# Kernel tuning notes

Hardware: AMD Instinct MI355X
Metric: run time of the kernel (lower is better)

The kernel has to match this reference:

```python
import jax, jax.numpy as jnp
import numpy as np

TEMPERATURE = 0.07


def setup_inputs() -> dict:
    key = jax.random.key(0)
    k1, k2 = jax.random.split(key)
    embeddings = jax.random.normal(k1, (8192, 256), dtype=jnp.float32)
    labels = jax.random.randint(k2, (8192,), 0, 1024, dtype=jnp.int64)
    return {"embeddings": embeddings, "labels": labels}


def reference(embeddings, labels):
    b = embeddings.shape[0]
    # L2 normalize rows (torch F.normalize uses eps=1e-12 clamp on the norm)
    norm = jnp.linalg.norm(embeddings, axis=1, keepdims=True)
    en = embeddings / jnp.maximum(norm, 1e-12)
    # [B, B] similarity scaled by temperature
    sim = jnp.matmul(en, en.T) / TEMPERATURE
    # log-softmax over rows (denominator includes the diagonal, as in the original)
    logp = jax.nn.log_softmax(sim, axis=1)
    # positive mask: same label, excluding self
    mask = (labels[:, None] == labels[None, :]) & ~jnp.eye(b, dtype=bool)
    pos_mask = mask.astype(logp.dtype)
    pos_count = pos_mask.sum(axis=1)
    pos_sum = -jnp.sum(logp * pos_mask, axis=1)
    pos_loss = jnp.where(pos_count > 0, pos_sum / jnp.maximum(pos_count, 1.0), 0.0)
    return pos_loss.mean()
```

## Files before the change

### kernel.cpp

```cpp
#include <hip/hip_runtime.h>
#include <hip/hip_bf16.h>

#define B_N 8192
#define D_K 256
#define BM  32
#define BN  128
#define JSPLIT 2
#define JSPAN (B_N / JSPLIT)
#define NTILE (JSPAN / BN)
#define INVT 14.285714285714286f

typedef __bf16 bf16x8 __attribute__((ext_vector_type(8)));
typedef float  f32x16 __attribute__((ext_vector_type(16)));

#define AS1 __attribute__((address_space(1)))
#define AS3 __attribute__((address_space(3)))

__device__ __forceinline__ unsigned short f32_to_bf16_rne(float f) {
    unsigned int u = __float_as_uint(f);
    unsigned int r = (u + 0x7FFFu + ((u >> 16) & 1u)) >> 16;
    return (unsigned short)r;
}

__global__ void zero_misc(float* out, int* hist) {
    if (threadIdx.x < 1024) hist[threadIdx.x] = 0;
    if (threadIdx.x == 0) out[0] = 0.0f;
}

__global__ void norm_kernel(const float* __restrict__ emb,
                            unsigned short* __restrict__ en,
                            const int* __restrict__ labels,
                            int* __restrict__ hist) {
    const int row = blockIdx.x;
    const int t   = threadIdx.x;
    float x  = emb[row * D_K + t];
    float ss = x * x;
    #pragma unroll
    for (int m = 32; m; m >>= 1) ss += __shfl_xor(ss, m, 64);
    __shared__ float wsum[4];
    if ((t & 63) == 0) wsum[t >> 6] = ss;
    __syncthreads();
    float tot = wsum[0] + wsum[1] + wsum[2] + wsum[3];
    float sc  = 1.0f / fmaxf(sqrtf(tot), 1e-12f);
    en[row * D_K + t] = f32_to_bf16_rne(x * sc);
    if (t == 0) atomicAdd(&hist[labels[row]], 1);
}

__launch_bounds__(256, 2)
__global__ void loss_kernel(const unsigned short* __restrict__ en,
                            const int* __restrict__ labels,
                            float* __restrict__ s_part,
                            float* __restrict__ ps_part) {
    __shared__ unsigned short Bls[BN * D_K];
    __shared__ int   Lls[BN];
    __shared__ float comb[2][4][BM];

    const int t  = threadIdx.x;
    const int l  = t & 63;
    const int w  = t >> 6;
    const int ir = l & 31;
    const int h  = l >> 5;

    const int b   = blockIdx.x;
    const int swz = (b & 7) * (gridDim.x >> 3) + (b >> 3);
    const int jsplit = swz >> 8;
    const int itile  = swz & 255;
    const int ibase  = itile * BM;
    const int j0base = jsplit * JSPAN;

    bf16x8 bi[16];
    {
        const unsigned short* ap = en + (size_t)(ibase + ir) * D_K + h * 8;
        #pragma unroll
        for (int ks = 0; ks < 16; ++ks)
            bi[ks] = *reinterpret_cast<const bf16x8*>(ap + ks * 16);
    }
    const int i_glob = ibase + ir;
    const int li = labels[i_glob];

    float s_acc = 0.0f, ps_acc = 0.0f;

    for (int it = 0; it < NTILE; ++it) {
        const int j0g = j0base + it * BN;

        __syncthreads();
        #pragma unroll
        for (int rd = 0; rd < 16; ++rd) {
            int c    = rd * 256 + t;
            int row  = c >> 5;
            int m16  = c & 31;
            int srcm = m16 ^ (row & 7);
            const unsigned short* g =
                en + (size_t)(j0g + row) * D_K + srcm * 8;
            __builtin_amdgcn_global_load_lds(
                (const AS1 void*)g,
                (AS3 void*)((unsigned short*)Bls + (size_t)c * 8), 16, 0, 0);
        }
        if (t < BN) Lls[t] = labels[j0g + t];
        __syncthreads();

        f32x16 acc;
        #pragma unroll
        for (int q = 0; q < 16; ++q) acc[q] = 0.0f;
        const int x = ir & 7;
        const char* arow = (const char*)Bls + (size_t)(w * 32 + ir) * 512;
        #pragma unroll
        for (int ks = 0; ks < 16; ++ks) {
            int chunk = ((ks << 1) | h) ^ x;
            const bf16x8 af =
                *reinterpret_cast<const bf16x8*>(arow + (chunk << 4));
            acc = __builtin_amdgcn_mfma_f32_32x32x16_bf16(af, bi[ks], acc,
                                                          0, 0, 0);
        }

        const bool dtile = (j0g == (ibase & ~(BN - 1)));
        if (dtile) {
            #pragma unroll
            for (int r = 0; r < 16; ++r) {
                int jl = w * 32 + (r & 3) + ((r >> 2) << 3) + (h << 2);
                int lj = Lls[jl];
                float dot = acc[r];
                s_acc += __expf(fmaf(dot, INVT, -INVT));
                bool mm = (lj == li) & ((j0g + jl) != i_glob);
                ps_acc += mm ? dot : 0.0f;
            }
        } else {
            #pragma unroll
            for (int r = 0; r < 16; ++r) {
                int jl = w * 32 + (r & 3) + ((r >> 2) << 3) + (h << 2);
                int lj = Lls[jl];
                float dot = acc[r];
                s_acc += __expf(fmaf(dot, INVT, -INVT));
                ps_acc += (lj == li) ? dot : 0.0f;
            }
        }
    }

    s_acc  += __shfl_xor(s_acc, 32, 64);
    ps_acc += __shfl_xor(ps_acc, 32, 64);
    if (h == 0) { comb[0][w][ir] = s_acc; comb[1][w][ir] = ps_acc; }
    __syncthreads();
    if (t < BM) {
        float st  = comb[0][0][t] + comb[0][1][t] + comb[0][2][t] + comb[0][3][t];
        float pst = comb[1][0][t] + comb[1][1][t] + comb[1][2][t] + comb[1][3][t];
        s_part[jsplit * B_N + ibase + t]  = st;
        ps_part[jsplit * B_N + ibase + t] = pst;
    }
}

__global__ void final_kernel(const float* __restrict__ s_part,
                             const float* __restrict__ ps_part,
                             const int* __restrict__ labels,
                             const int* __restrict__ hist,
                             float* __restrict__ out) {
    int i = blockIdx.x * 256 + threadIdx.x;
    float s  = s_part[i] + s_part[B_N + i];
    float ps = ps_part[i] + ps_part[B_N + i];
    int pc = hist[labels[i]] - 1;
    float lse = INVT + __logf(s);
    float loss = (pc > 0) ? (lse - ps * INVT / (float)pc) : 0.0f;
    #pragma unroll
    for (int m = 1; m < 64; m <<= 1) loss += __shfl_xor(loss, m, 64);
    __shared__ float ws4[4];
    if ((threadIdx.x & 63) == 0) ws4[threadIdx.x >> 6] = loss;
    __syncthreads();
    if (threadIdx.x == 0)
        atomicAdd(out, (ws4[0] + ws4[1] + ws4[2] + ws4[3]) * (1.0f / B_N));
}

extern "C" void kernel_launch(void* const* d_in, const int* in_sizes, int n_in,
                              void* d_out, int out_size, void* d_ws, size_t ws_size,
                              hipStream_t stream) {
    const float* emb    = (const float*)d_in[0];
    const int*   labels = (const int*)d_in[1];
    float*       out    = (float*)d_out;

    unsigned short* en  = (unsigned short*)d_ws;
    float* s_part  = (float*)((char*)d_ws + (size_t)B_N * D_K * 2);
    float* ps_part = s_part + JSPLIT * B_N;
    int*   hist    = (int*)(ps_part + JSPLIT * B_N);

    hipLaunchKernelGGL(zero_misc, dim3(1), dim3(1024), 0, stream, out, hist);
    hipLaunchKernelGGL(norm_kernel, dim3(B_N), dim3(D_K), 0, stream,
                       emb, en, labels, hist);
    hipLaunchKernelGGL(loss_kernel, dim3(256 * JSPLIT), dim3(256), 0, stream,
                       en, labels, s_part, ps_part);
    hipLaunchKernelGGL(final_kernel, dim3(B_N / 256), dim3(256), 0, stream,
                       s_part, ps_part, labels, hist, out);
}
```

Baseline: 131.1 us.

## Compute positive-pair sums via per-class centroid sums and enlarge loss tile

Replaces the per-pair positive-mask accumulation in the main loop with an algebraic identity: per-class sums of normalized embeddings are built with float atomics in the norm kernel, and each row's positive sum becomes dot(e_i, C_label) minus the self dot. The loss kernel then only accumulates the softmax denominator, using exp2 with a folded constant, and the i-tile grows to 64 rows with four j-splits so each loaded B tile feeds two MFMA passes. The norm kernel is also vectorized to four rows per block. The cost is 256 float atomics per row into the class-sum matrix, plus a zeroing pass over that matrix and rounding differences between the bf16 embeddings and the fp32 class sums.

```diff
diff --git a/kernel.cpp b/kernel.cpp
--- a/kernel.cpp
+++ b/kernel.cpp
@@ -3,15 +3,18 @@
 
 #define B_N 8192
 #define D_K 256
-#define BM  32
+#define BM  64
 #define BN  128
-#define JSPLIT 2
+#define JSPLIT 4
 #define JSPAN (B_N / JSPLIT)
 #define NTILE (JSPAN / BN)
+#define NCLS 1024
 #define INVT 14.285714285714286f
+#define C1   20.60992907f
 
 typedef __bf16 bf16x8 __attribute__((ext_vector_type(8)));
 typedef float  f32x16 __attribute__((ext_vector_type(16)));
+typedef float  f32x4  __attribute__((ext_vector_type(4)));
 
 #define AS1 __attribute__((address_space(1)))
 #define AS3 __attribute__((address_space(3)))
@@ -21,151 +24,155 @@
     unsigned int r = (u + 0x7FFFu + ((u >> 16) & 1u)) >> 16;
     return (unsigned short)r;
 }
+__device__ __forceinline__ float bf16_to_f32(unsigned short u) {
+    return __uint_as_float(((unsigned int)u) << 16);
+}
 
-__global__ void zero_misc(float* out, int* hist) {
-    if (threadIdx.x < 1024) hist[threadIdx.x] = 0;
-    if (threadIdx.x == 0) out[0] = 0.0f;
+__global__ void zero_kernel(float* __restrict__ out, int* __restrict__ hist,
+                            float* __restrict__ Cmat) {
+    int g = blockIdx.x * 256 + threadIdx.x;
+    Cmat[g] = 0.0f;
+    if (g < NCLS) hist[g] = 0;
+    if (g == 0) out[0] = 0.0f;
 }
 
 __global__ void norm_kernel(const float* __restrict__ emb,
+                            const int* __restrict__ labels,
                             unsigned short* __restrict__ en,
-                            const int* __restrict__ labels,
+                            float* __restrict__ Cmat,
                             int* __restrict__ hist) {
-    const int row = blockIdx.x;
-    const int t   = threadIdx.x;
-    float x  = emb[row * D_K + t];
-    float ss = x * x;
+    const int t = threadIdx.x;
+    const int w = t >> 6, l = t & 63;
+    const int row = blockIdx.x * 4 + w;
+    f32x4 x = *reinterpret_cast<const f32x4*>(emb + (size_t)row * D_K + l * 4);
+    float ss = x[0]*x[0] + x[1]*x[1] + x[2]*x[2] + x[3]*x[3];
     #pragma unroll
-    for (int m = 32; m; m >>= 1) ss += __shfl_xor(ss, m, 64);
-    __shared__ float wsum[4];
-    if ((t & 63) == 0) wsum[t >> 6] = ss;
-    __syncthreads();
-    float tot = wsum[0] + wsum[1] + wsum[2] + wsum[3];
-    float sc  = 1.0f / fmaxf(sqrtf(tot), 1e-12f);
-    en[row * D_K + t] = f32_to_bf16_rne(x * sc);
-    if (t == 0) atomicAdd(&hist[labels[row]], 1);
+    for (int m = 1; m < 64; m <<= 1) ss += __shfl_xor(ss, m, 64);
+    float sc = 1.0f / fmaxf(sqrtf(ss), 1e-12f);
+    const int lab = labels[row];
+    float xn[4];
+    ushort4 o;
+    #pragma unroll
+    for (int k = 0; k < 4; ++k) xn[k] = x[k] * sc;
+    o.x = f32_to_bf16_rne(xn[0]); o.y = f32_to_bf16_rne(xn[1]);
+    o.z = f32_to_bf16_rne(xn[2]); o.w = f32_to_bf16_rne(xn[3]);
+    *reinterpret_cast<ushort4*>(en + (size_t)row * D_K + l * 4) = o;
+    #pragma unroll
+    for (int k = 0; k < 4; ++k)
+        atomicAdd(&Cmat[lab * D_K + l * 4 + k], xn[k]);
+    if (l == 0) atomicAdd(&hist[lab], 1);
 }
 
 __launch_bounds__(256, 2)
 __global__ void loss_kernel(const unsigned short* __restrict__ en,
-                            const int* __restrict__ labels,
-                            float* __restrict__ s_part,
-                            float* __restrict__ ps_part) {
-    __shared__ unsigned short Bls[BN * D_K];
-    __shared__ int   Lls[BN];
-    __shared__ float comb[2][4][BM];
+                            float* __restrict__ s_part) {
+    __shared__ __align__(16) unsigned short Bls[BN * D_K];
+    __shared__ float comb[4][32];
 
     const int t  = threadIdx.x;
     const int l  = t & 63;
     const int w  = t >> 6;
     const int ir = l & 31;
     const int h  = l >> 5;
+    const int jh = w & 1;
+    const int ih = w >> 1;
 
-    const int b   = blockIdx.x;
-    const int swz = (b & 7) * (gridDim.x >> 3) + (b >> 3);
-    const int jsplit = swz >> 8;
-    const int itile  = swz & 255;
+    const int b      = blockIdx.x;
+    const int swz    = (b & 7) * 64 + (b >> 3);
+    const int jsplit = swz >> 7;
+    const int itile  = swz & 127;
     const int ibase  = itile * BM;
-    const int j0base = jsplit * JSPAN;
 
     bf16x8 bi[16];
     {
-        const unsigned short* ap = en + (size_t)(ibase + ir) * D_K + h * 8;
+        const unsigned short* ap =
+            en + (size_t)(ibase + ih * 32 + ir) * D_K + h * 8;
         #pragma unroll
         for (int ks = 0; ks < 16; ++ks)
             bi[ks] = *reinterpret_cast<const bf16x8*>(ap + ks * 16);
     }
-    const int i_glob = ibase + ir;
-    const int li = labels[i_glob];
 
-    float s_acc = 0.0f, ps_acc = 0.0f;
+    const int srcm = (t & 31) ^ ((t >> 5) & 7);
+    const unsigned short* gb = en + (size_t)(jsplit * JSPAN) * D_K
+                                  + (size_t)(t >> 5) * D_K + srcm * 8;
+    char* lds_base = (char*)Bls + t * 16;
+    const char* abase = (const char*)Bls + (size_t)(jh * 64 + ir) * 512;
+    const int xr = (ir & 7) << 4;
+
+    float s_acc = 0.0f;
 
     for (int it = 0; it < NTILE; ++it) {
-        const int j0g = j0base + it * BN;
-
         __syncthreads();
         #pragma unroll
         for (int rd = 0; rd < 16; ++rd) {
-            int c    = rd * 256 + t;
-            int row  = c >> 5;
-            int m16  = c & 31;
-            int srcm = m16 ^ (row & 7);
-            const unsigned short* g =
-                en + (size_t)(j0g + row) * D_K + srcm * 8;
             __builtin_amdgcn_global_load_lds(
-                (const AS1 void*)g,
-                (AS3 void*)((unsigned short*)Bls + (size_t)c * 8), 16, 0, 0);
+                (const AS1 void*)(gb + rd * (8 * D_K)),
+                (AS3 void*)(lds_base + rd * 4096), 16, 0, 0);
         }
-        if (t < BN) Lls[t] = labels[j0g + t];
+        gb += (size_t)BN * D_K;
         __syncthreads();
 
-        f32x16 acc;
         #pragma unroll
-        for (int q = 0; q < 16; ++q) acc[q] = 0.0f;
-        const int x = ir & 7;
-        const char* arow = (const char*)Bls + (size_t)(w * 32 + ir) * 512;
-        #pragma unroll
-        for (int ks = 0; ks < 16; ++ks) {
-            int chunk = ((ks << 1) | h) ^ x;
-            const bf16x8 af =
-                *reinterpret_cast<const bf16x8*>(arow + (chunk << 4));
-            acc = __builtin_amdgcn_mfma_f32_32x32x16_bf16(af, bi[ks], acc,
-                                                          0, 0, 0);
-        }
-
-        const bool dtile = (j0g == (ibase & ~(BN - 1)));
-        if (dtile) {
+        for (int jg2 = 0; jg2 < 2; ++jg2) {
+            f32x16 acc;
             #pragma unroll
-            for (int r = 0; r < 16; ++r) {
-                int jl = w * 32 + (r & 3) + ((r >> 2) << 3) + (h << 2);
-                int lj = Lls[jl];
-                float dot = acc[r];
-                s_acc += __expf(fmaf(dot, INVT, -INVT));
-                bool mm = (lj == li) & ((j0g + jl) != i_glob);
-                ps_acc += mm ? dot : 0.0f;
+            for (int q = 0; q < 16; ++q) acc[q] = 0.0f;
+            const char* arow = abase + jg2 * (32 * 512);
+            #pragma unroll
+            for (int ks = 0; ks < 16; ++ks) {
+                const bf16x8 af = *reinterpret_cast<const bf16x8*>(
+                    arow + ((((ks << 1) | h) << 4) ^ xr));
+                acc = __builtin_amdgcn_mfma_f32_32x32x16_bf16(af, bi[ks], acc,
+                                                              0, 0, 0);
             }
-        } else {
             #pragma unroll
-            for (int r = 0; r < 16; ++r) {
-                int jl = w * 32 + (r & 3) + ((r >> 2) << 3) + (h << 2);
-                int lj = Lls[jl];
-                float dot = acc[r];
-                s_acc += __expf(fmaf(dot, INVT, -INVT));
-                ps_acc += (lj == li) ? dot : 0.0f;
-            }
+            for (int q = 0; q < 16; ++q)
+                s_acc += exp2f(fmaf(acc[q], C1, -C1));
         }
     }
 
-    s_acc  += __shfl_xor(s_acc, 32, 64);
-    ps_acc += __shfl_xor(ps_acc, 32, 64);
-    if (h == 0) { comb[0][w][ir] = s_acc; comb[1][w][ir] = ps_acc; }
+    s_acc += __shfl_xor(s_acc, 32, 64);
+    if (h == 0) comb[w][ir] = s_acc;
     __syncthreads();
     if (t < BM) {
-        float st  = comb[0][0][t] + comb[0][1][t] + comb[0][2][t] + comb[0][3][t];
-        float pst = comb[1][0][t] + comb[1][1][t] + comb[1][2][t] + comb[1][3][t];
-        s_part[jsplit * B_N + ibase + t]  = st;
-        ps_part[jsplit * B_N + ibase + t] = pst;
+        float sv = comb[(t >> 5) * 2][t & 31] + comb[(t >> 5) * 2 + 1][t & 31];
+        s_part[jsplit * B_N + ibase + t] = sv;
     }
 }
 
-__global__ void final_kernel(const float* __restrict__ s_part,
-                             const float* __restrict__ ps_part,
+__global__ void final_kernel(const unsigned short* __restrict__ en,
                              const int* __restrict__ labels,
+                             const float* __restrict__ s_part,
+                             const float* __restrict__ Cmat,
                              const int* __restrict__ hist,
                              float* __restrict__ out) {
-    int i = blockIdx.x * 256 + threadIdx.x;
-    float s  = s_part[i] + s_part[B_N + i];
-    float ps = ps_part[i] + ps_part[B_N + i];
-    int pc = hist[labels[i]] - 1;
-    float lse = INVT + __logf(s);
-    float loss = (pc > 0) ? (lse - ps * INVT / (float)pc) : 0.0f;
+    const int t = threadIdx.x, w = t >> 6, l = t & 63;
+    const int i = blockIdx.x * 4 + w;
+    const int lab = labels[i];
+    ushort4 eu = *reinterpret_cast<const ushort4*>(en + (size_t)i * D_K + l * 4);
+    f32x4  c4  = *reinterpret_cast<const f32x4*>(Cmat + lab * D_K + l * 4);
+    float e0 = bf16_to_f32(eu.x), e1 = bf16_to_f32(eu.y),
+          e2 = bf16_to_f32(eu.z), e3 = bf16_to_f32(eu.w);
+    float dot  = e0 * c4[0] + e1 * c4[1] + e2 * c4[2] + e3 * c4[3];
+    float self = e0 * e0 + e1 * e1 + e2 * e2 + e3 * e3;
     #pragma unroll
-    for (int m = 1; m < 64; m <<= 1) loss += __shfl_xor(loss, m, 64);
-    __shared__ float ws4[4];
-    if ((threadIdx.x & 63) == 0) ws4[threadIdx.x >> 6] = loss;
+    for (int m = 1; m < 64; m <<= 1) {
+        dot  += __shfl_xor(dot, m, 64);
+        self += __shfl_xor(self, m, 64);
+    }
+    __shared__ float part[4];
+    if (l == 0) {
+        float s = s_part[i] + s_part[B_N + i] + s_part[2 * B_N + i]
+                + s_part[3 * B_N + i];
+        int pc = hist[lab] - 1;
+        float lse  = INVT + logf(s);
+        float ps   = (dot - self) * INVT;
+        float loss = (pc > 0) ? (lse - ps / (float)pc) : 0.0f;
+        part[w] = loss;
+    }
     __syncthreads();
-    if (threadIdx.x == 0)
-        atomicAdd(out, (ws4[0] + ws4[1] + ws4[2] + ws4[3]) * (1.0f / B_N));
+    if (t == 0)
+        atomicAdd(out, (part[0] + part[1] + part[2] + part[3]) * (1.0f / B_N));
 }
 
 extern "C" void kernel_launch(void* const* d_in, const int* in_sizes, int n_in,
@@ -175,16 +182,17 @@
     const int*   labels = (const int*)d_in[1];
     float*       out    = (float*)d_out;
 
-    unsigned short* en  = (unsigned short*)d_ws;
-    float* s_part  = (float*)((char*)d_ws + (size_t)B_N * D_K * 2);
-    float* ps_part = s_part + JSPLIT * B_N;
-    int*   hist    = (int*)(ps_part + JSPLIT * B_N);
+    unsigned short* en = (unsigned short*)d_ws;
+    float* s_part = (float*)((char*)d_ws + (size_t)B_N * D_K * 2);
+    int*   hist   = (int*)(s_part + JSPLIT * B_N);
+    float* Cmat   = (float*)(hist + NCLS);
 
-    hipLaunchKernelGGL(zero_misc, dim3(1), dim3(1024), 0, stream, out, hist);
-    hipLaunchKernelGGL(norm_kernel, dim3(B_N), dim3(D_K), 0, stream,
-                       emb, en, labels, hist);
-    hipLaunchKernelGGL(loss_kernel, dim3(256 * JSPLIT), dim3(256), 0, stream,
-                       en, labels, s_part, ps_part);
-    hipLaunchKernelGGL(final_kernel, dim3(B_N / 256), dim3(256), 0, stream,
-                       s_part, ps_part, labels, hist, out);
+    hipLaunchKernelGGL(zero_kernel, dim3(NCLS * D_K / 256), dim3(256), 0,
+                       stream, out, hist, Cmat);
+    hipLaunchKernelGGL(norm_kernel, dim3(B_N / 4), dim3(256), 0, stream,
+                       emb, labels, en, Cmat, hist);
+    hipLaunchKernelGGL(loss_kernel, dim3(128 * JSPLIT), dim3(256), 0, stream,
+                       en, s_part);
+    hipLaunchKernelGGL(final_kernel, dim3(B_N / 4), dim3(256), 0, stream,
+                       en, labels, s_part, Cmat, hist, out);
 }
```

Result: slower. 166.3 us (+26.8%).
